# Kernel optimization log

Hardware: AMD Instinct MI355X
Metric: run time of the kernel (lower is better)

Reference implementation:

```python
import jax, jax.numpy as jnp
import numpy as np

B, L = 16, 2048
D_MODEL, D_INNER, D_STATE, DT_RANK, D_CONV = 128, 256, 16, 8, 4
N_LAYERS, N_CLASSES = 4, 5
EPS = 1e-5


def setup_inputs() -> dict:
    key = jax.random.key(0)
    ks = jax.random.split(key, 12)
    rn = lambda k, shape, s=0.02: jax.random.normal(k, shape, jnp.float32) * s
    A_log = jnp.log(jnp.arange(1, D_STATE + 1, dtype=jnp.float32))  # S4D-real init
    return dict(
        x=jax.random.normal(ks[0], (B, L, 12), jnp.float32),
        enc_w=rn(ks[1], (D_MODEL, 12), 0.1),
        enc_b=jnp.zeros((D_MODEL,), jnp.float32),
        norm_w=jnp.ones((N_LAYERS, D_MODEL), jnp.float32),
        in_proj_w=rn(ks[2], (N_LAYERS, 2 * D_INNER, D_MODEL)),
        conv_w=rn(ks[3], (N_LAYERS, D_INNER, D_CONV), 0.1),
        conv_b=jnp.zeros((N_LAYERS, D_INNER), jnp.float32),
        x_proj_w=rn(ks[4], (N_LAYERS, DT_RANK + 2 * D_STATE, D_INNER)),
        dt_proj_w=rn(ks[5], (N_LAYERS, D_INNER, DT_RANK), 0.1),
        dt_proj_b=rn(ks[6], (N_LAYERS, D_INNER), 0.1),
        A_log=jnp.broadcast_to(A_log, (N_LAYERS, D_INNER, D_STATE)) + 0.0,
        Dp=jnp.ones((N_LAYERS, D_INNER), jnp.float32),
        out_proj_w=rn(ks[7], (N_LAYERS, D_MODEL, D_INNER)),
        norm_f_w=jnp.ones((D_MODEL,), jnp.float32),
        cls_w=rn(ks[8], (N_CLASSES, D_MODEL), 0.05),
        cls_b=jnp.zeros((N_CLASSES,), jnp.float32),
    )


def rmsnorm(x, w):
    return x * jax.lax.rsqrt(jnp.mean(x * x, axis=-1, keepdims=True) + EPS) * w


def causal_depthwise_conv(x, w, b):
    # x: [b, l, di]; w: [di, k]; causal (left) padding, groups=di
    xc = x.transpose(0, 2, 1)  # [b, di, l]
    y = jax.lax.conv_general_dilated(
        xc, w[:, None, :], window_strides=(1,), padding=[(D_CONV - 1, 0)],
        dimension_numbers=("NCH", "OIH", "NCH"), feature_group_count=D_INNER)
    return (y + b[None, :, None]).transpose(0, 2, 1)


def selective_scan(u, delta, A, Bm, Cm, Dv):
    # u, delta: [b,l,di]; A: [di,n]; Bm, Cm: [b,l,n]; Dv: [di]
    dA = jnp.exp(jnp.einsum("bld,dn->bldn", delta, A))          # [b,l,di,n]
    dBu = jnp.einsum("bld,bln,bld->bldn", delta, Bm, u)          # [b,l,di,n]

    def step(h, inp):
        dA_t, dBu_t, C_t = inp
        h = dA_t * h + dBu_t                                     # [b,di,n]
        y = jnp.einsum("bdn,bn->bd", h, C_t)
        return h, y

    h0 = jnp.zeros((u.shape[0], u.shape[2], A.shape[1]), u.dtype)
    xs = (dA.transpose(1, 0, 2, 3), dBu.transpose(1, 0, 2, 3), Cm.transpose(1, 0, 2))
    _, ys = jax.lax.scan(step, h0, xs)
    return ys.transpose(1, 0, 2) + u * Dv


def mamba_block(x, in_w, cw, cb, xp_w, dt_w, dt_b, A_log_i, D_i, out_w):
    xz = jnp.einsum("bld,ed->ble", x, in_w)                      # [b,l,2*di]
    xm, z = xz[..., :D_INNER], xz[..., D_INNER:]
    xm = jax.nn.silu(causal_depthwise_conv(xm, cw, cb))
    x_dbl = jnp.einsum("bld,ed->ble", xm, xp_w)                  # [b,l,dt_rank+2n]
    dt = x_dbl[..., :DT_RANK]
    Bm = x_dbl[..., DT_RANK:DT_RANK + D_STATE]
    Cm = x_dbl[..., DT_RANK + D_STATE:]
    delta = jax.nn.softplus(jnp.einsum("blr,dr->bld", dt, dt_w) + dt_b)
    A = -jnp.exp(A_log_i)
    y = selective_scan(xm, delta, A, Bm, Cm, D_i)
    y = y * jax.nn.silu(z)
    return jnp.einsum("bld,ed->ble", y, out_w)


def reference(x, enc_w, enc_b, norm_w, in_proj_w, conv_w, conv_b, x_proj_w,
              dt_proj_w, dt_proj_b, A_log, Dp, out_proj_w, norm_f_w, cls_w, cls_b):
    h = jnp.einsum("blc,dc->bld", x, enc_w) + enc_b               # conv1d k=1 encoder
    for i in range(N_LAYERS):
        h = mamba_block(rmsnorm(h, norm_w[i]), in_proj_w[i], conv_w[i], conv_b[i],
                        x_proj_w[i], dt_proj_w[i], dt_proj_b[i], A_log[i], Dp[i],
                        out_proj_w[i]) + h
    h = rmsnorm(h, norm_f_w)
    pooled = jnp.mean(h, axis=1)                                  # AdaptiveAvgPool1d(1)
    return pooled @ cls_w.T + cls_b                               # [B, n_classes]
```

## Files before the change

### kernel.cpp

```cpp
#include <hip/hip_runtime.h>
#include <hip/hip_bf16.h>
#include <cstddef>

#define BB 16
#define LL 2048
#define DM 128
#define DI 256
#define DS 16
#define MP (BB*LL)
#define NSEG 64
#define SEGLEN (LL/NSEG)
#define YSTR 264
#define XSTR 40

typedef __attribute__((ext_vector_type(8))) short bf16x8;
typedef __attribute__((ext_vector_type(4))) short bf16x4s;
typedef __attribute__((ext_vector_type(8))) unsigned int ux8;
typedef __attribute__((ext_vector_type(4))) float f32x4;
typedef __hip_bfloat16 bf16;
typedef unsigned int uint;

__device__ inline void bf16split(float x, bf16& h, bf16& l) {
  h = __float2bfloat16(x);
  l = __float2bfloat16(x - __bfloat162float(h));
}
__device__ inline float bf2f(bf16 v) { return __bfloat162float(v); }
__device__ inline void split_bits2(float x, short& hs, short& ls) {
  bf16 hb = __float2bfloat16(x);
  bf16 lb = __float2bfloat16(x - __bfloat162float(hb));
  hs = *(short*)&hb;
  ls = *(short*)&lb;
}
__device__ inline short bfbits(float x) {
  bf16 b = __float2bfloat16(x);
  return *(short*)&b;
}
__device__ inline float sigm(float x) {
  return __builtin_amdgcn_rcpf(1.f + __expf(-x));
}
__device__ inline uint pk2(short h, short l) {
  return (uint)(unsigned short)h | ((uint)(unsigned short)l << 16);
}
__device__ inline uint pack_hl(float x) {
  short hs, ls; split_bits2(x, hs, ls);
  return pk2(hs, ls);
}
__device__ inline float unpack_hl(uint w) {
  return __uint_as_float(w << 16) + __uint_as_float(w & 0xffff0000u);
}

__global__ __launch_bounds__(256, 4) void gemm_inproj(
    const bf16* __restrict__ Ah, const bf16* __restrict__ Al,
    const bf16* __restrict__ Wh, const bf16* __restrict__ Wl,
    uint* __restrict__ xm_pk, uint* __restrict__ zs_pk) {
  int tid = threadIdx.x;
  int wave = tid >> 6, lane = tid & 63;
  int r16 = lane & 15, quad = lane >> 4;
  int bid = blockIdx.x;
  int nh = bid & 1, mb = bid >> 1;
  int m0 = mb * 32;
  int n0 = nh * 256 + wave * 64;
  size_t arow[2], brow[4];
#pragma unroll
  for (int i = 0; i < 2; i++)
    arow[i] = (size_t)(m0 + i * 16 + r16) * DM + quad * 8;
#pragma unroll
  for (int j = 0; j < 4; j++)
    brow[j] = (size_t)(n0 + j * 16 + r16) * DM + quad * 8;
  f32x4 acc[2][4] = {};
#pragma unroll
  for (int kk = 0; kk < 4; kk++) {
    int ko = kk * 32;
    bf16x8 ah[2], al[2], bh[4], bl[4];
#pragma unroll
    for (int i = 0; i < 2; i++) {
      ah[i] = *(const bf16x8*)(Ah + arow[i] + ko);
      al[i] = *(const bf16x8*)(Al + arow[i] + ko);
    }
#pragma unroll
    for (int j = 0; j < 4; j++) {
      bh[j] = *(const bf16x8*)(Wh + brow[j] + ko);
      bl[j] = *(const bf16x8*)(Wl + brow[j] + ko);
    }
#pragma unroll
    for (int i = 0; i < 2; i++)
#pragma unroll
      for (int j = 0; j < 4; j++) {
        acc[i][j] = __builtin_amdgcn_mfma_f32_16x16x32_bf16(ah[i], bh[j], acc[i][j], 0, 0, 0);
        acc[i][j] = __builtin_amdgcn_mfma_f32_16x16x32_bf16(ah[i], bl[j], acc[i][j], 0, 0, 0);
        acc[i][j] = __builtin_amdgcn_mfma_f32_16x16x32_bf16(al[i], bh[j], acc[i][j], 0, 0, 0);
      }
  }
  bool isz = (n0 >= 256);
  uint* dst = isz ? zs_pk : xm_pk;
  int cb = n0 & 255;
#pragma unroll
  for (int i = 0; i < 2; i++)
#pragma unroll
    for (int j = 0; j < 4; j++)
#pragma unroll
      for (int r = 0; r < 4; r++) {
        int row = m0 + i * 16 + quad * 4 + r;
        int col = cb + j * 16 + r16;
        float v = acc[i][j][r];
        if (isz) v *= sigm(v);
        dst[(size_t)row * DI + col] = pack_hl(v);
      }
}

__global__ __launch_bounds__(256, 2) void gemm_conv(
    const uint* __restrict__ xm_pk,
    const bf16* __restrict__ Wh, const bf16* __restrict__ Wl,
    const float* __restrict__ cw, const float* __restrict__ cb,
    float* __restrict__ C, uint* __restrict__ u_pk) {
  __shared__ float scw[DI * 4 + DI];
  int tid = threadIdx.x;
  {
    float4 w4 = *(const float4*)(cw + tid * 4);
    *(float4*)(scw + tid * 4) = w4;
    scw[DI * 4 + tid] = cb[tid];
  }
  __syncthreads();
  int wave = tid >> 6, lane = tid & 63;
  int r16 = lane & 15, quad = lane >> 4;
  int m0 = blockIdx.x * 64 + wave * 16;
  int m = m0 + r16;
  int l = m & (LL - 1);
  size_t rb[4]; float msk[3];
#pragma unroll
  for (int t = 0; t < 3; t++) {
    msk[t] = (l >= (3 - t)) ? 1.f : 0.f;
    int mr = m - 3 + t; if (mr < 0) mr = 0;
    rb[t] = (size_t)mr * DI;
  }
  rb[3] = (size_t)m * DI;
  size_t brow[3];
#pragma unroll
  for (int j = 0; j < 3; j++)
    brow[j] = (size_t)(j * 16 + r16) * DI + quad * 8;
  f32x4 acc[3] = {};
#pragma unroll
  for (int kk = 0; kk < 8; kk++) {
    int ko = quad * 8 + kk * 32;
    bf16x8 ah, al, bh[3], bl[3];
    ux8 xv[4];
#pragma unroll
    for (int t = 0; t < 4; t++)
      xv[t] = *(const ux8*)(xm_pk + rb[t] + ko);
#pragma unroll
    for (int e = 0; e < 8; e++) {
      int k = ko + e;
      float x0 = unpack_hl(xv[0][e]) * msk[0];
      float x1 = unpack_hl(xv[1][e]) * msk[1];
      float x2 = unpack_hl(xv[2][e]) * msk[2];
      float x3 = unpack_hl(xv[3][e]);
      float c0 = scw[DI * 4 + k] + scw[k*4]*x0 + scw[k*4+1]*x1 + scw[k*4+2]*x2 + scw[k*4+3]*x3;
      float u = c0 * sigm(c0);
      short hs, ls; split_bits2(u, hs, ls);
      ah[e] = hs; al[e] = ls;
    }
    {
      size_t g = rb[3] + ko;
      uint4 p0, p1;
      p0.x = pk2(ah[0], al[0]); p0.y = pk2(ah[1], al[1]);
      p0.z = pk2(ah[2], al[2]); p0.w = pk2(ah[3], al[3]);
      p1.x = pk2(ah[4], al[4]); p1.y = pk2(ah[5], al[5]);
      p1.z = pk2(ah[6], al[6]); p1.w = pk2(ah[7], al[7]);
      *(uint4*)(u_pk + g) = p0;
      *(uint4*)(u_pk + g + 4) = p1;
    }
#pragma unroll
    for (int j = 0; j < 3; j++) {
      bh[j] = *(const bf16x8*)(Wh + brow[j] + kk * 32);
      bl[j] = *(const bf16x8*)(Wl + brow[j] + kk * 32);
    }
#pragma unroll
    for (int j = 0; j < 3; j++) {
      acc[j] = __builtin_amdgcn_mfma_f32_16x16x32_bf16(ah, bh[j], acc[j], 0, 0, 0);
      acc[j] = __builtin_amdgcn_mfma_f32_16x16x32_bf16(ah, bl[j], acc[j], 0, 0, 0);
      acc[j] = __builtin_amdgcn_mfma_f32_16x16x32_bf16(al, bh[j], acc[j], 0, 0, 0);
    }
  }
#pragma unroll
  for (int j = 0; j < 3; j++)
#pragma unroll
    for (int r = 0; r < 4; r++) {
      int row = m0 + quad * 4 + r;
      int col = j * 16 + r16;
      C[(size_t)row * 64 + col] = acc[j][r];
    }
}

__global__ __launch_bounds__(256) void encoder_kernel(const float* __restrict__ x,
    const float* __restrict__ ew, const float* __restrict__ eb,
    float* __restrict__ h) {
  int idx = blockIdx.x * 256 + threadIdx.x;
  int d = idx & 127, m = idx >> 7;
  float acc = eb[d];
#pragma unroll
  for (int c = 0; c < 12; c++) acc += x[m * 12 + c] * ew[d * 12 + c];
  h[idx] = acc;
}

__global__ void split_w(const float* __restrict__ src, bf16* __restrict__ hi,
                        bf16* __restrict__ lo, int n) {
  int i = blockIdx.x * 256 + threadIdx.x;
  if (i < n) bf16split(src[i], hi[i], lo[i]);
}

__global__ void split_w_pad(const float* __restrict__ src, bf16* __restrict__ hi,
                            bf16* __restrict__ lo) {
  int i = blockIdx.x * 256 + threadIdx.x;
  int l = i >> 14, rem = i & 16383, r = rem >> 8, k = rem & 255;
  float v = (r < 40) ? src[l * 10240 + r * 256 + k] : 0.f;
  bf16split(v, hi[i], lo[i]);
}

__global__ __launch_bounds__(256) void rmsnorm_kernel(const float* __restrict__ x,
    const float* __restrict__ w, bf16* __restrict__ oh, bf16* __restrict__ ol) {
  int lane = threadIdx.x & 63;
  int pos = blockIdx.x * 4 + (threadIdx.x >> 6);
  const float* row = x + (size_t)pos * DM;
  float v0 = row[lane], v1 = row[lane + 64];
  float ss = v0 * v0 + v1 * v1;
#pragma unroll
  for (int off = 1; off < 64; off <<= 1) ss += __shfl_xor(ss, off);
  float sc = rsqrtf(ss * (1.f / DM) + 1e-5f);
  float a = v0 * sc * w[lane], b = v1 * sc * w[lane + 64];
  size_t o = (size_t)pos * DM;
  bf16split(a, oh[o + lane], ol[o + lane]);
  bf16split(b, oh[o + lane + 64], ol[o + lane + 64]);
}

__device__ inline float softplus_f(float a) {
  float r = __logf(1.f + __expf(a));
  return a > 15.f ? a : r;
}

__device__ inline void make_powers(float r, float* rp) {
  rp[0] = r;
#pragma unroll
  for (int n = 1; n < 16; n++) {
    int a = (n + 1) >> 1, b = (n + 1) - a;
    rp[n] = rp[a - 1] * rp[b - 1];
  }
}

__device__ inline bool a_is_integer(const float* A_log, int d) {
  bool ok = true;
#pragma unroll
  for (int n = 0; n < DS; n++) {
    float Ad = -__expf(A_log[d * DS + n]);
    ok = ok && (fabsf(Ad + (float)(n + 1)) < 1e-3f);
  }
  return ok;
}

__device__ inline void load_sx(float* sx, const float* xdbl, size_t rbase, int tid) {
#pragma unroll
  for (int j = 0; j < 2; j++) {
    int idx = j * 256 + tid;
    if (idx < 320) {
      int row = idx / 10, c = idx % 10;
      *(float4*)(sx + row * XSTR + c * 4) = *(const float4*)(xdbl + rbase + row * 64 + c * 4);
    }
  }
}

template<bool FAST>
__device__ inline void scan1_body(int s, int b, int d, const float* sx,
    const uint* __restrict__ u_pk,
    const float* __restrict__ dtw, const float* __restrict__ dtb,
    const float* __restrict__ A_log,
    float* __restrict__ sega, float* __restrict__ segh) {
  float wdt[8];
#pragma unroll
  for (int j = 0; j < 8; j++) wdt[j] = dtw[d * 8 + j];
  float bdt = dtb[d];
  float h[DS];
#pragma unroll
  for (int n = 0; n < DS; n++) h[n] = 0.f;
  float R = 1.f;
  float ap[DS];
  if (!FAST) {
#pragma unroll
    for (int n = 0; n < DS; n++) ap[n] = 1.f;
  }
  size_t base = (size_t)b * LL + (size_t)s * SEGLEN;
  const uint* up = u_pk + base * DI + d;
  uint ub = *up;
#pragma unroll 4
  for (int t = 0; t < SEGLEN; t++) {
    up += DI;
    uint ub_next = *up;
    const float* xr = sx + t * XSTR;
    float dt = bdt;
#pragma unroll
    for (int j = 0; j < 8; j++) dt += xr[j] * wdt[j];
    float dl = softplus_f(dt);
    float u = unpack_hl(ub);
    float du = dl * u;
    if (FAST) {
      float rp[DS];
      make_powers(__expf(-dl), rp);
      R *= rp[0];
#pragma unroll
      for (int n = 0; n < DS; n++) h[n] = fmaf(rp[n], h[n], du * xr[8 + n]);
    } else {
#pragma unroll
      for (int n = 0; n < DS; n++) {
        float dA = __expf(dl * (-__expf(A_log[d * DS + n])));
        h[n] = fmaf(dA, h[n], du * xr[8 + n]);
        ap[n] *= dA;
      }
    }
    ub = ub_next;
  }
  if (FAST) make_powers(R, ap);
  size_t o = ((size_t)s * 4096 + b * 256 + d) * DS;
#pragma unroll
  for (int j = 0; j < 4; j++) {
    *(float4*)(sega + o + 4 * j) = make_float4(ap[4*j], ap[4*j+1], ap[4*j+2], ap[4*j+3]);
    *(float4*)(segh + o + 4 * j) = make_float4(h[4*j], h[4*j+1], h[4*j+2], h[4*j+3]);
  }
}

__global__ __launch_bounds__(256, 6) void scan_phase1(
    const uint* __restrict__ u_pk, const float* __restrict__ xdbl,
    const float* __restrict__ dtw, const float* __restrict__ dtb,
    const float* __restrict__ A_log,
    float* __restrict__ sega, float* __restrict__ segh) {
  __shared__ float sx[SEGLEN * XSTR];
  int s = blockIdx.x, b = blockIdx.y, d = threadIdx.x;
  size_t rbase = ((size_t)b * LL + (size_t)s * SEGLEN) * 64;
  load_sx(sx, xdbl, rbase, d);
  __syncthreads();
  if (a_is_integer(A_log, d))
    scan1_body<true>(s, b, d, sx, u_pk, dtw, dtb, A_log, sega, segh);
  else
    scan1_body<false>(s, b, d, sx, u_pk, dtw, dtb, A_log, sega, segh);
}

__global__ __launch_bounds__(256) void scan_combine(float* __restrict__ sega,
    const float* __restrict__ segh) {
  int g = blockIdx.x * 256 + threadIdx.x;
  size_t off = (size_t)(g >> 2) * 16 + (g & 3) * 4;
  float4 h0 = make_float4(0.f, 0.f, 0.f, 0.f);
  for (int s = 0; s < NSEG; s++) {
    size_t q = (size_t)s * 65536 + off;
    float4 a = *(float4*)(sega + q);
    float4 hh = *(float4*)(segh + q);
    *(float4*)(sega + q) = h0;
    h0.x = a.x * h0.x + hh.x;
    h0.y = a.y * h0.y + hh.y;
    h0.z = a.z * h0.z + hh.z;
    h0.w = a.w * h0.w + hh.w;
  }
}

template<bool FAST>
__device__ inline void scan2_to_lds(int s, int b, int d, const float* sx,
    const uint* __restrict__ u_pk, const uint* __restrict__ zs_pk,
    const float* __restrict__ dtw, const float* __restrict__ dtb,
    const float* __restrict__ A_log, const float* __restrict__ Dp,
    const float* __restrict__ sega, short* __restrict__ ybuf) {
  float wdt[8];
#pragma unroll
  for (int j = 0; j < 8; j++) wdt[j] = dtw[d * 8 + j];
  float bdt = dtb[d];
  float h[DS];
  size_t o = ((size_t)s * 4096 + b * 256 + d) * DS;
#pragma unroll
  for (int n = 0; n < DS; n++) h[n] = sega[o + n];
  float Dd = Dp[d];
  size_t base = (size_t)b * LL + (size_t)s * SEGLEN;
  const uint* up = u_pk + base * DI + d;
  const uint* zp = zs_pk + base * DI + d;
  uint ub = *up, zb = *zp;
#pragma unroll 4
  for (int t = 0; t < SEGLEN; t++) {
    up += DI; zp += DI;
    uint ub_next = *up;
    uint zb_next = *zp;
    const float* xr = sx + t * XSTR;
    float dt = bdt;
#pragma unroll
    for (int j = 0; j < 8; j++) dt += xr[j] * wdt[j];
    float dl = softplus_f(dt);
    float u = unpack_hl(ub);
    float du = dl * u;
    float acc = 0.f;
    if (FAST) {
      float rp[DS];
      make_powers(__expf(-dl), rp);
#pragma unroll
      for (int n = 0; n < DS; n++) {
        h[n] = fmaf(rp[n], h[n], du * xr[8 + n]);
        acc = fmaf(h[n], xr[24 + n], acc);
      }
    } else {
#pragma unroll
      for (int n = 0; n < DS; n++) {
        float dA = __expf(dl * (-__expf(A_log[d * DS + n])));
        h[n] = fmaf(dA, h[n], du * xr[8 + n]);
        acc = fmaf(h[n], xr[24 + n], acc);
      }
    }
    float zs = unpack_hl(zb);
    float yv = (acc + u * Dd) * zs;
    ybuf[t * YSTR + d] = bfbits(yv);
    ub = ub_next; zb = zb_next;
  }
}

__global__ __launch_bounds__(256, 6) void scan2_outproj(
    const uint* __restrict__ u_pk, const uint* __restrict__ zs_pk,
    const float* __restrict__ xdbl, const float* __restrict__ dtw,
    const float* __restrict__ dtb, const float* __restrict__ A_log,
    const float* __restrict__ Dp, const float* __restrict__ sega,
    const bf16* __restrict__ Wh, const bf16* __restrict__ Wl,
    float* __restrict__ hbuf, const float* __restrict__ nw,
    float* __restrict__ of, bf16* __restrict__ oh, bf16* __restrict__ ol) {
  __shared__ float sx[SEGLEN * XSTR];
  __shared__ short ybuf[32 * YSTR];
  int s = blockIdx.x, b = blockIdx.y;
  int tid = threadIdx.x, d = tid;
  size_t rbase = ((size_t)b * LL + (size_t)s * SEGLEN) * 64;
  load_sx(sx, xdbl, rbase, tid);
  __syncthreads();
  if (a_is_integer(A_log, d))
    scan2_to_lds<true>(s, b, d, sx, u_pk, zs_pk, dtw, dtb, A_log, Dp, sega, ybuf);
  else
    scan2_to_lds<false>(s, b, d, sx, u_pk, zs_pk, dtw, dtb, A_log, Dp, sega, ybuf);
  __syncthreads();
  int wave = tid >> 6, lane = tid & 63;
  int r16 = lane & 15, quad = lane >> 4;
  int n0 = wave * 32;
  size_t brow[2];
#pragma unroll
  for (int j = 0; j < 2; j++)
    brow[j] = (size_t)(n0 + j * 16 + r16) * DI + quad * 8;
  f32x4 acc[2][2] = {};
#pragma unroll
  for (int kk = 0; kk < 8; kk++) {
    int k0 = quad * 8 + kk * 32;
    bf16x8 ah[2], bh[2], bl[2];
#pragma unroll
    for (int i = 0; i < 2; i++)
      ah[i] = *(const bf16x8*)(ybuf + (i * 16 + r16) * YSTR + k0);
#pragma unroll
    for (int j = 0; j < 2; j++) {
      bh[j] = *(const bf16x8*)(Wh + brow[j] + kk * 32);
      bl[j] = *(const bf16x8*)(Wl + brow[j] + kk * 32);
    }
#pragma unroll
    for (int i = 0; i < 2; i++)
#pragma unroll
      for (int j = 0; j < 2; j++) {
        acc[i][j] = __builtin_amdgcn_mfma_f32_16x16x32_bf16(ah[i], bh[j], acc[i][j], 0, 0, 0);
        acc[i][j] = __builtin_amdgcn_mfma_f32_16x16x32_bf16(ah[i], bl[j], acc[i][j], 0, 0, 0);
      }
  }
  __syncthreads();
  float* tile = (float*)ybuf;
#pragma unroll
  for (int i = 0; i < 2; i++)
#pragma unroll
    for (int j = 0; j < 2; j++)
#pragma unroll
      for (int r = 0; r < 4; r++) {
        int rl = i * 16 + quad * 4 + r;
        int col = n0 + j * 16 + r16;
        tile[rl * 132 + col] = acc[i][j][r];
      }
  __syncthreads();
  size_t mbase = (size_t)b * LL + (size_t)s * SEGLEN;
#pragma unroll
  for (int it = 0; it < 4; it++) {
    int idx = it * 256 + tid;
    int row = idx >> 5, c4 = idx & 31;
    size_t g = (mbase + row) * DM + c4 * 4;
    float4 hv = *(float4*)(hbuf + g);
    const float* tp = tile + row * 132 + c4 * 4;
    float4 v = make_float4(tp[0] + hv.x, tp[1] + hv.y, tp[2] + hv.z, tp[3] + hv.w);
    *(float4*)(hbuf + g) = v;
    float ss = v.x * v.x + v.y * v.y + v.z * v.z + v.w * v.w;
    ss += __shfl_xor(ss, 1);
    ss += __shfl_xor(ss, 2);
    ss += __shfl_xor(ss, 4);
    ss += __shfl_xor(ss, 8);
    ss += __shfl_xor(ss, 16);
    float sc = rsqrtf(ss * (1.f / DM) + 1e-5f);
    float4 w4 = *(const float4*)(nw + c4 * 4);
    float n0v = v.x * sc * w4.x, n1v = v.y * sc * w4.y;
    float n2v = v.z * sc * w4.z, n3v = v.w * sc * w4.w;
    if (of) *(float4*)(of + g) = make_float4(n0v, n1v, n2v, n3v);
    short h0s, l0s, h1s, l1s, h2s, l2s, h3s, l3s;
    split_bits2(n0v, h0s, l0s); split_bits2(n1v, h1s, l1s);
    split_bits2(n2v, h2s, l2s); split_bits2(n3v, h3s, l3s);
    bf16x4s hb, lb;
    hb[0] = h0s; hb[1] = h1s; hb[2] = h2s; hb[3] = h3s;
    lb[0] = l0s; lb[1] = l1s; lb[2] = l2s; lb[3] = l3s;
    *(bf16x4s*)(oh + g) = hb;
    *(bf16x4s*)(ol + g) = lb;
  }
}

__global__ __launch_bounds__(256) void pool_partial(const float* __restrict__ fn,
    float* __restrict__ partial) {
  __shared__ float red[256];
  int b = blockIdx.x, c = blockIdx.y;
  int tid = threadIdx.x;
  int d = tid & 127, rp_ = tid >> 7;
  float s = 0.f;
  size_t base = (size_t)b * LL + c * 256;
  for (int i = 0; i < 128; i++) {
    int row = i * 2 + rp_;
    s += fn[(base + row) * DM + d];
  }
  red[tid] = s;
  __syncthreads();
  if (tid < 128) partial[((size_t)b * 8 + c) * 128 + tid] = red[tid] + red[tid + 128];
}

__global__ void pool_reduce(const float* __restrict__ partial,
    float* __restrict__ pooled) {
  int idx = blockIdx.x * 256 + threadIdx.x;
  int b = idx >> 7, d = idx & 127;
  float s = 0.f;
#pragma unroll
  for (int c = 0; c < 8; c++) s += partial[((size_t)b * 8 + c) * 128 + d];
  pooled[idx] = s * (1.f / LL);
}

__global__ void cls_kernel(const float* __restrict__ pooled,
    const float* __restrict__ cw, const float* __restrict__ cb,
    float* __restrict__ out) {
  int t = threadIdx.x;
  if (t < 80) {
    int b = t / 5, c = t % 5;
    float acc = cb[c];
    for (int d = 0; d < DM; d++) acc += pooled[b * DM + d] * cw[c * DM + d];
    out[t] = acc;
  }
}

extern "C" void kernel_launch(void* const* d_in, const int* in_sizes, int n_in,
                              void* d_out, int out_size, void* d_ws, size_t ws_size,
                              hipStream_t stream) {
  const float* x         = (const float*)d_in[0];
  const float* enc_w     = (const float*)d_in[1];
  const float* enc_b     = (const float*)d_in[2];
  const float* norm_w    = (const float*)d_in[3];
  const float* in_proj_w = (const float*)d_in[4];
  const float* conv_w    = (const float*)d_in[5];
  const float* conv_b    = (const float*)d_in[6];
  const float* x_proj_w  = (const float*)d_in[7];
  const float* dt_proj_w = (const float*)d_in[8];
  const float* dt_proj_b = (const float*)d_in[9];
  const float* A_log     = (const float*)d_in[10];
  const float* Dp        = (const float*)d_in[11];
  const float* out_proj_w= (const float*)d_in[12];
  const float* norm_f_w  = (const float*)d_in[13];
  const float* cls_w     = (const float*)d_in[14];
  const float* cls_b     = (const float*)d_in[15];
  float* out = (float*)d_out;

  float* ws = (float*)d_ws;
  float* h       = ws;
  float* xdbl    = ws + 4194304;
  float* sega    = ws + 6291456;
  float* segh    = ws + 10485760;
  uint*  zs_pk   = (uint*)(ws + 14680064);
  uint*  u_pk    = (uint*)(ws + 23068672);
  uint*  xm_pk   = (uint*)(ws + 31457280);
  float* partial = ws + 39845888;
  float* pooled  = ws + 39862272;
  bf16* u0     = (bf16*)(ws + 39864320);
  bf16* xn_hi  = u0;
  bf16* xn_lo  = u0 + 4194304;
  bf16* wip_hi = u0 + 8388608;
  bf16* wip_lo = wip_hi + 262144;
  bf16* wxp_hi = wip_lo + 262144;
  bf16* wxp_lo = wxp_hi + 65536;
  bf16* wop_hi = wxp_lo + 65536;
  bf16* wop_lo = wop_hi + 131072;
  float* fnorm = (float*)xm_pk;

  split_w<<<1024, 256, 0, stream>>>(in_proj_w, wip_hi, wip_lo, 262144);
  split_w_pad<<<256, 256, 0, stream>>>(x_proj_w, wxp_hi, wxp_lo);
  split_w<<<512, 256, 0, stream>>>(out_proj_w, wop_hi, wop_lo, 131072);

  encoder_kernel<<<MP * DM / 256, 256, 0, stream>>>(x, enc_w, enc_b, h);
  rmsnorm_kernel<<<MP / 4, 256, 0, stream>>>(h, norm_w, xn_hi, xn_lo);

  for (int i = 0; i < 4; i++) {
    gemm_inproj<<<MP / 16, 256, 0, stream>>>(xn_hi, xn_lo,
        wip_hi + i * 65536, wip_lo + i * 65536, xm_pk, zs_pk);
    gemm_conv<<<MP / 64, 256, 0, stream>>>(xm_pk,
        wxp_hi + i * 16384, wxp_lo + i * 16384,
        conv_w + i * DI * 4, conv_b + i * DI, xdbl, u_pk);
    scan_phase1<<<dim3(NSEG, BB), 256, 0, stream>>>(u_pk, xdbl,
        dt_proj_w + i * 2048, dt_proj_b + i * DI, A_log + i * DI * DS, sega, segh);
    scan_combine<<<64, 256, 0, stream>>>(sega, segh);
    scan2_outproj<<<dim3(NSEG, BB), 256, 0, stream>>>(u_pk, zs_pk, xdbl,
        dt_proj_w + i * 2048, dt_proj_b + i * DI, A_log + i * DI * DS,
        Dp + i * DI, sega, wop_hi + i * 32768, wop_lo + i * 32768, h,
        (i < 3) ? norm_w + (i + 1) * DM : norm_f_w,
        (i < 3) ? nullptr : fnorm, xn_hi, xn_lo);
  }

  pool_partial<<<dim3(BB, 8), 256, 0, stream>>>(fnorm, partial);
  pool_reduce<<<8, 256, 0, stream>>>(partial, pooled);
  cls_kernel<<<1, 128, 0, stream>>>(pooled, cls_w, cls_b, out);
}
```

Baseline: 778.2 us.

## Fuse in_proj GEMM with causal conv and x_proj GEMM via LDS halo

Merges the in_proj GEMM and the conv+x_proj GEMM into one kernel. Each block computes a 32-row tile plus a 16-row halo for the x half, keeps xm in shared memory for the depthwise conv, and feeds the conv output from LDS into the x_proj MFMA. This removes the xm_pk global write and read and one launch per layer. In exchange it recomputes the halo rows, uses much more LDS, allows fewer blocks per CU, and leaves the x_proj stage unevenly split across waves.

```diff
diff --git a/kernel.cpp b/kernel.cpp
--- a/kernel.cpp
+++ b/kernel.cpp
@@ -49,70 +49,16 @@
   return __uint_as_float(w << 16) + __uint_as_float(w & 0xffff0000u);
 }
 
-__global__ __launch_bounds__(256, 4) void gemm_inproj(
+__global__ __launch_bounds__(256, 2) void gemm_inproj_conv(
     const bf16* __restrict__ Ah, const bf16* __restrict__ Al,
     const bf16* __restrict__ Wh, const bf16* __restrict__ Wl,
-    uint* __restrict__ xm_pk, uint* __restrict__ zs_pk) {
-  int tid = threadIdx.x;
-  int wave = tid >> 6, lane = tid & 63;
-  int r16 = lane & 15, quad = lane >> 4;
-  int bid = blockIdx.x;
-  int nh = bid & 1, mb = bid >> 1;
-  int m0 = mb * 32;
-  int n0 = nh * 256 + wave * 64;
-  size_t arow[2], brow[4];
-#pragma unroll
-  for (int i = 0; i < 2; i++)
-    arow[i] = (size_t)(m0 + i * 16 + r16) * DM + quad * 8;
-#pragma unroll
-  for (int j = 0; j < 4; j++)
-    brow[j] = (size_t)(n0 + j * 16 + r16) * DM + quad * 8;
-  f32x4 acc[2][4] = {};
-#pragma unroll
-  for (int kk = 0; kk < 4; kk++) {
-    int ko = kk * 32;
-    bf16x8 ah[2], al[2], bh[4], bl[4];
-#pragma unroll
-    for (int i = 0; i < 2; i++) {
-      ah[i] = *(const bf16x8*)(Ah + arow[i] + ko);
-      al[i] = *(const bf16x8*)(Al + arow[i] + ko);
-    }
-#pragma unroll
-    for (int j = 0; j < 4; j++) {
-      bh[j] = *(const bf16x8*)(Wh + brow[j] + ko);
-      bl[j] = *(const bf16x8*)(Wl + brow[j] + ko);
-    }
-#pragma unroll
-    for (int i = 0; i < 2; i++)
-#pragma unroll
-      for (int j = 0; j < 4; j++) {
-        acc[i][j] = __builtin_amdgcn_mfma_f32_16x16x32_bf16(ah[i], bh[j], acc[i][j], 0, 0, 0);
-        acc[i][j] = __builtin_amdgcn_mfma_f32_16x16x32_bf16(ah[i], bl[j], acc[i][j], 0, 0, 0);
-        acc[i][j] = __builtin_amdgcn_mfma_f32_16x16x32_bf16(al[i], bh[j], acc[i][j], 0, 0, 0);
-      }
-  }
-  bool isz = (n0 >= 256);
-  uint* dst = isz ? zs_pk : xm_pk;
-  int cb = n0 & 255;
-#pragma unroll
-  for (int i = 0; i < 2; i++)
-#pragma unroll
-    for (int j = 0; j < 4; j++)
-#pragma unroll
-      for (int r = 0; r < 4; r++) {
-        int row = m0 + i * 16 + quad * 4 + r;
-        int col = cb + j * 16 + r16;
-        float v = acc[i][j][r];
-        if (isz) v *= sigm(v);
-        dst[(size_t)row * DI + col] = pack_hl(v);
-      }
-}
-
-__global__ __launch_bounds__(256, 2) void gemm_conv(
-    const uint* __restrict__ xm_pk,
-    const bf16* __restrict__ Wh, const bf16* __restrict__ Wl,
+    const bf16* __restrict__ Xh, const bf16* __restrict__ Xl,
     const float* __restrict__ cw, const float* __restrict__ cb,
-    float* __restrict__ C, uint* __restrict__ u_pk) {
+    uint* __restrict__ zs_pk, uint* __restrict__ u_pk,
+    float* __restrict__ C) {
+  __shared__ uint  xmb[35 * 260];
+  __shared__ short ubh[32 * 264];
+  __shared__ short ubl[32 * 264];
   __shared__ float scw[DI * 4 + DI];
   int tid = threadIdx.x;
   {
@@ -120,75 +66,134 @@
     *(float4*)(scw + tid * 4) = w4;
     scw[DI * 4 + tid] = cb[tid];
   }
-  __syncthreads();
   int wave = tid >> 6, lane = tid & 63;
   int r16 = lane & 15, quad = lane >> 4;
-  int m0 = blockIdx.x * 64 + wave * 16;
-  int m = m0 + r16;
-  int l = m & (LL - 1);
-  size_t rb[4]; float msk[3];
-#pragma unroll
-  for (int t = 0; t < 3; t++) {
-    msk[t] = (l >= (3 - t)) ? 1.f : 0.f;
-    int mr = m - 3 + t; if (mr < 0) mr = 0;
-    rb[t] = (size_t)mr * DI;
-  }
-  rb[3] = (size_t)m * DI;
-  size_t brow[3];
-#pragma unroll
-  for (int j = 0; j < 3; j++)
-    brow[j] = (size_t)(j * 16 + r16) * DI + quad * 8;
-  f32x4 acc[3] = {};
-#pragma unroll
-  for (int kk = 0; kk < 8; kk++) {
-    int ko = quad * 8 + kk * 32;
-    bf16x8 ah, al, bh[3], bl[3];
-    ux8 xv[4];
-#pragma unroll
-    for (int t = 0; t < 4; t++)
-      xv[t] = *(const ux8*)(xm_pk + rb[t] + ko);
-#pragma unroll
-    for (int e = 0; e < 8; e++) {
-      int k = ko + e;
-      float x0 = unpack_hl(xv[0][e]) * msk[0];
-      float x1 = unpack_hl(xv[1][e]) * msk[1];
-      float x2 = unpack_hl(xv[2][e]) * msk[2];
-      float x3 = unpack_hl(xv[3][e]);
-      float c0 = scw[DI * 4 + k] + scw[k*4]*x0 + scw[k*4+1]*x1 + scw[k*4+2]*x2 + scw[k*4+3]*x3;
+  int m0 = blockIdx.x * 32;
+
+  size_t arow[3];
+#pragma unroll
+  for (int rt = 0; rt < 3; rt++) {
+    int rg = m0 - 16 + rt * 16 + r16;
+    if (rg < 0) rg = 0;
+    arow[rt] = (size_t)rg * DM + quad * 8;
+  }
+  size_t browx[4], browz[4];
+#pragma unroll
+  for (int ct = 0; ct < 4; ct++) {
+    browx[ct] = (size_t)(wave * 64 + ct * 16 + r16) * DM + quad * 8;
+    browz[ct] = (size_t)(256 + wave * 64 + ct * 16 + r16) * DM + quad * 8;
+  }
+  f32x4 accx[3][4] = {};
+  f32x4 accz[2][4] = {};
+#pragma unroll
+  for (int kk = 0; kk < 4; kk++) {
+    int ko = kk * 32;
+    bf16x8 ah[3], al[3], bxh[4], bxl[4], bzh[4], bzl[4];
+#pragma unroll
+    for (int rt = 0; rt < 3; rt++) {
+      ah[rt] = *(const bf16x8*)(Ah + arow[rt] + ko);
+      al[rt] = *(const bf16x8*)(Al + arow[rt] + ko);
+    }
+#pragma unroll
+    for (int ct = 0; ct < 4; ct++) {
+      bxh[ct] = *(const bf16x8*)(Wh + browx[ct] + ko);
+      bxl[ct] = *(const bf16x8*)(Wl + browx[ct] + ko);
+      bzh[ct] = *(const bf16x8*)(Wh + browz[ct] + ko);
+      bzl[ct] = *(const bf16x8*)(Wl + browz[ct] + ko);
+    }
+#pragma unroll
+    for (int rt = 0; rt < 3; rt++)
+#pragma unroll
+      for (int ct = 0; ct < 4; ct++) {
+        accx[rt][ct] = __builtin_amdgcn_mfma_f32_16x16x32_bf16(ah[rt], bxh[ct], accx[rt][ct], 0, 0, 0);
+        accx[rt][ct] = __builtin_amdgcn_mfma_f32_16x16x32_bf16(ah[rt], bxl[ct], accx[rt][ct], 0, 0, 0);
+        accx[rt][ct] = __builtin_amdgcn_mfma_f32_16x16x32_bf16(al[rt], bxh[ct], accx[rt][ct], 0, 0, 0);
+      }
+#pragma unroll
+    for (int rz = 0; rz < 2; rz++)
+#pragma unroll
+      for (int ct = 0; ct < 4; ct++) {
+        accz[rz][ct] = __builtin_amdgcn_mfma_f32_16x16x32_bf16(ah[rz + 1], bzh[ct], accz[rz][ct], 0, 0, 0);
+        accz[rz][ct] = __builtin_amdgcn_mfma_f32_16x16x32_bf16(ah[rz + 1], bzl[ct], accz[rz][ct], 0, 0, 0);
+        accz[rz][ct] = __builtin_amdgcn_mfma_f32_16x16x32_bf16(al[rz + 1], bzh[ct], accz[rz][ct], 0, 0, 0);
+      }
+  }
+#pragma unroll
+  for (int rz = 0; rz < 2; rz++)
+#pragma unroll
+    for (int ct = 0; ct < 4; ct++)
+#pragma unroll
+      for (int r = 0; r < 4; r++) {
+        int row = m0 + rz * 16 + quad * 4 + r;
+        int col = wave * 64 + ct * 16 + r16;
+        float v = accz[rz][ct][r];
+        v *= sigm(v);
+        zs_pk[(size_t)row * DI + col] = pack_hl(v);
+      }
+#pragma unroll
+  for (int rt = 0; rt < 3; rt++)
+#pragma unroll
+    for (int ct = 0; ct < 4; ct++)
+#pragma unroll
+      for (int r = 0; r < 4; r++) {
+        int lidx = rt * 16 + quad * 4 + r - 13;
+        if (lidx >= 0)
+          xmb[lidx * 260 + wave * 64 + ct * 16 + r16] = pack_hl(accx[rt][ct][r]);
+      }
+  __syncthreads();
+
+  {
+    int d = tid;
+    float w0 = scw[d * 4], w1 = scw[d * 4 + 1], w2 = scw[d * 4 + 2], w3 = scw[d * 4 + 3];
+    float bias = scw[DI * 4 + d];
+    float xa = unpack_hl(xmb[0 * 260 + d]);
+    float xb = unpack_hl(xmb[1 * 260 + d]);
+    float xc = unpack_hl(xmb[2 * 260 + d]);
+    int lbase = m0 & (LL - 1);
+#pragma unroll 4
+    for (int t = 0; t < 32; t++) {
+      float xd = unpack_hl(xmb[(t + 3) * 260 + d]);
+      int l = lbase + t;
+      float x0 = xa * ((l >= 3) ? 1.f : 0.f);
+      float x1 = xb * ((l >= 2) ? 1.f : 0.f);
+      float x2 = xc * ((l >= 1) ? 1.f : 0.f);
+      float c0 = bias + w0 * x0 + w1 * x1 + w2 * x2 + w3 * xd;
       float u = c0 * sigm(c0);
       short hs, ls; split_bits2(u, hs, ls);
-      ah[e] = hs; al[e] = ls;
-    }
-    {
-      size_t g = rb[3] + ko;
-      uint4 p0, p1;
-      p0.x = pk2(ah[0], al[0]); p0.y = pk2(ah[1], al[1]);
-      p0.z = pk2(ah[2], al[2]); p0.w = pk2(ah[3], al[3]);
-      p1.x = pk2(ah[4], al[4]); p1.y = pk2(ah[5], al[5]);
-      p1.z = pk2(ah[6], al[6]); p1.w = pk2(ah[7], al[7]);
-      *(uint4*)(u_pk + g) = p0;
-      *(uint4*)(u_pk + g + 4) = p1;
-    }
-#pragma unroll
-    for (int j = 0; j < 3; j++) {
-      bh[j] = *(const bf16x8*)(Wh + brow[j] + kk * 32);
-      bl[j] = *(const bf16x8*)(Wl + brow[j] + kk * 32);
-    }
-#pragma unroll
-    for (int j = 0; j < 3; j++) {
-      acc[j] = __builtin_amdgcn_mfma_f32_16x16x32_bf16(ah, bh[j], acc[j], 0, 0, 0);
-      acc[j] = __builtin_amdgcn_mfma_f32_16x16x32_bf16(ah, bl[j], acc[j], 0, 0, 0);
-      acc[j] = __builtin_amdgcn_mfma_f32_16x16x32_bf16(al, bh[j], acc[j], 0, 0, 0);
-    }
-  }
-#pragma unroll
-  for (int j = 0; j < 3; j++)
-#pragma unroll
-    for (int r = 0; r < 4; r++) {
-      int row = m0 + quad * 4 + r;
-      int col = j * 16 + r16;
-      C[(size_t)row * 64 + col] = acc[j][r];
-    }
+      u_pk[(size_t)(m0 + t) * DI + d] = pk2(hs, ls);
+      ubh[t * 264 + d] = hs;
+      ubl[t * 264 + d] = ls;
+      xa = xb; xb = xc; xc = xd;
+    }
+  }
+  __syncthreads();
+
+  {
+    int rt0 = (wave == 3) ? 1 : 0;
+    int ct0 = (wave == 0) ? 0 : (wave == 1) ? 1 : (wave == 2) ? 2 : 0;
+#pragma unroll 1
+    for (int tt = 0; tt < 2; tt++) {
+      int rt, ct;
+      if (tt == 0) { rt = rt0; ct = ct0; }
+      else { if (wave >= 2) break; rt = 1; ct = wave + 1; }
+      f32x4 a2 = {};
+#pragma unroll
+      for (int kk = 0; kk < 8; kk++) {
+        int k0 = quad * 8 + kk * 32;
+        bf16x8 ahh = *(const bf16x8*)(ubh + (rt * 16 + r16) * 264 + k0);
+        bf16x8 alo = *(const bf16x8*)(ubl + (rt * 16 + r16) * 264 + k0);
+        size_t br = (size_t)(ct * 16 + r16) * DI + quad * 8 + kk * 32;
+        bf16x8 bhh = *(const bf16x8*)(Xh + br);
+        bf16x8 blo = *(const bf16x8*)(Xl + br);
+        a2 = __builtin_amdgcn_mfma_f32_16x16x32_bf16(ahh, bhh, a2, 0, 0, 0);
+        a2 = __builtin_amdgcn_mfma_f32_16x16x32_bf16(ahh, blo, a2, 0, 0, 0);
+        a2 = __builtin_amdgcn_mfma_f32_16x16x32_bf16(alo, bhh, a2, 0, 0, 0);
+      }
+#pragma unroll
+      for (int r = 0; r < 4; r++)
+        C[(size_t)(m0 + rt * 16 + quad * 4 + r) * 64 + ct * 16 + r16] = a2[r];
+    }
+  }
 }
 
 __global__ __launch_bounds__(256) void encoder_kernel(const float* __restrict__ x,
@@ -595,11 +600,11 @@
   rmsnorm_kernel<<<MP / 4, 256, 0, stream>>>(h, norm_w, xn_hi, xn_lo);
 
   for (int i = 0; i < 4; i++) {
-    gemm_inproj<<<MP / 16, 256, 0, stream>>>(xn_hi, xn_lo,
-        wip_hi + i * 65536, wip_lo + i * 65536, xm_pk, zs_pk);
-    gemm_conv<<<MP / 64, 256, 0, stream>>>(xm_pk,
+    gemm_inproj_conv<<<MP / 32, 256, 0, stream>>>(xn_hi, xn_lo,
+        wip_hi + i * 65536, wip_lo + i * 65536,
         wxp_hi + i * 16384, wxp_lo + i * 16384,
-        conv_w + i * DI * 4, conv_b + i * DI, xdbl, u_pk);
+        conv_w + i * DI * 4, conv_b + i * DI,
+        zs_pk, u_pk, xdbl);
     scan_phase1<<<dim3(NSEG, BB), 256, 0, stream>>>(u_pk, xdbl,
         dt_proj_w + i * 2048, dt_proj_b + i * DI, A_log + i * DI * DS, sega, segh);
     scan_combine<<<64, 256, 0, stream>>>(sega, segh);
```

Result: faster. 701.0 us (-9.9%).
